# Kernel tuning notes

Measured on AMD Instinct MI355X. Metric: run time of the kernel, lower is better.

The kernel has to match this reference:

```python
import jax, jax.numpy as jnp
import numpy as np

K = 64          # tagset size (len(tag_to_ix))
START = 62      # start_tag_id
STOP = 63       # stop_tag_id
NEG = -10000.0


def setup_inputs() -> dict:
    key = jax.random.key(0)
    k1, k2, k3 = jax.random.split(key, 3)
    B, T = 1024, 512
    feats = jax.random.normal(k1, (B, T, K), dtype=jnp.float32)
    tags = jax.random.randint(k2, (B, T), 0, K, dtype=jnp.int32)
    # learned transition matrix; transitions[i, j] = score of moving from tag j to tag i
    transitions = jax.random.normal(k3, (K, K), dtype=jnp.float32)
    transitions = transitions.at[START, :].set(NEG).at[:, STOP].set(NEG)
    return {"feats": feats, "tags": tags, "transitions": transitions}


def reference(feats, tags, transitions):
    B, T, _ = feats.shape
    # log_alpha init: -10000 everywhere except start tag (matches torch code; feats[:,0] unused)
    alpha0 = jnp.full((B, K), NEG, dtype=feats.dtype).at[:, START].set(0.0)

    def step(alpha, feat_t):
        # alpha: [B, K]; new_alpha[b, i] = lse_j(transitions[i, j] + alpha[b, j]) + feat_t[b, i]
        new_alpha = jax.nn.logsumexp(transitions[None, :, :] + alpha[:, None, :], axis=-1) + feat_t
        return new_alpha, None

    feats_seq = jnp.transpose(feats[:, 1:, :], (1, 0, 2))  # [T-1, B, K]
    alpha, _ = jax.lax.scan(step, alpha0, feats_seq)
    forward_score = jax.nn.logsumexp(alpha, axis=-1)  # [B]

    # gold path score: sum_t transitions[tags[t], tags[t-1]] + feats[t, tags[t]], t = 1..T-1
    trans_score = transitions[tags[:, 1:], tags[:, :-1]].sum(axis=1)  # [B]
    emit_score = jnp.take_along_axis(feats[:, 1:, :], tags[:, 1:, None], axis=2)[..., 0].sum(axis=1)  # [B]
    gold_score = trans_score + emit_score

    return jnp.mean(forward_score - gold_score)
```

## Files before the change

kernel.cpp:

```cpp
#include <hip/hip_runtime.h>


#define BB 1024
#define TT 512
#define KK 64
#define START_TAG 62

#define RLF(v, l) __uint_as_float((unsigned)__builtin_amdgcn_readlane((int)__float_as_uint(v), (l)))

__global__ __launch_bounds__(128, 2) void crf_fwdbwd_kernel(
    const float* __restrict__ feats,
    const int*   __restrict__ tags,
    const float* __restrict__ trans,
    float*       __restrict__ diff)
{
  const int lane = threadIdx.x & 63;
  const int wv   = threadIdx.x >> 6;
  const int b    = blockIdx.x;

  __shared__ float ysh[KK];
  __shared__ float gs_sh;
  __shared__ int   esumB_sh;

  const float* fb = feats + (size_t)b * TT * KK + lane;

  float beta = 0.0f;
  int   esumA = 0;

  if (wv == 0) {
    float4 e4[16];
    {
      const float4* trow = (const float4*)(trans + lane * KK);
      #pragma unroll
      for (int jc = 0; jc < 16; ++jc) {
        float4 tv = trow[jc];
        e4[jc] = make_float4(__expf(tv.x), __expf(tv.y),
                             __expf(tv.z), __expf(tv.w));
      }
    }

    float upf[5];
    #pragma unroll
    for (int d = 0; d < 5; ++d) upf[d] = fb[(size_t)(1 + d) * KK];

    beta = (lane == START_TAG) ? 1.0f : 0.0f;
    float f_cur = __expf(upf[0]);

    for (int g = 0; g < 51; ++g) {
      #pragma unroll
      for (int d = 0; d < 5; ++d) {
        const int t = 1 + g * 5 + d;

        float4 a0 = {0.f, 0.f, 0.f, 0.f};
        float4 a1 = {0.f, 0.f, 0.f, 0.f};
        #pragma unroll
        for (int jc = 0; jc < 16; jc += 2) {
          a0.x = fmaf(e4[jc].x,     RLF(beta, 4*jc + 0), a0.x);
          a0.y = fmaf(e4[jc].y,     RLF(beta, 4*jc + 1), a0.y);
          a0.z = fmaf(e4[jc].z,     RLF(beta, 4*jc + 2), a0.z);
          a0.w = fmaf(e4[jc].w,     RLF(beta, 4*jc + 3), a0.w);
          a1.x = fmaf(e4[jc + 1].x, RLF(beta, 4*jc + 4), a1.x);
          a1.y = fmaf(e4[jc + 1].y, RLF(beta, 4*jc + 5), a1.y);
          a1.z = fmaf(e4[jc + 1].z, RLF(beta, 4*jc + 6), a1.z);
          a1.w = fmaf(e4[jc + 1].w, RLF(beta, 4*jc + 7), a1.w);
        }
        float z = ((a0.x + a1.x) + (a0.y + a1.y)) +
                  ((a0.z + a1.z) + (a0.w + a1.w));

        int tn = t + 5; if (tn > 255) tn = 255;
        upf[d] = fb[(size_t)tn * KK];

        unsigned zb = (unsigned)__builtin_amdgcn_readlane((int)__float_as_uint(z), 0);
        float s = __uint_as_float(0x7F000000u - (zb & 0x7F800000u));
        esumA += (int)((zb >> 23) & 0xFFu) - 127;
        beta = (z * f_cur) * s;

        f_cur = __expf(upf[(d + 1 < 5) ? d + 1 : 0]);
      }
    }
  } else {
    float4 et4[16];
    #pragma unroll
    for (int jc = 0; jc < 16; ++jc) {
      et4[jc].x = __expf(trans[(4*jc + 0) * KK + lane]);
      et4[jc].y = __expf(trans[(4*jc + 1) * KK + lane]);
      et4[jc].z = __expf(trans[(4*jc + 2) * KK + lane]);
      et4[jc].w = __expf(trans[(4*jc + 3) * KK + lane]);
    }

    float upf[4];
    #pragma unroll
    for (int d = 0; d < 4; ++d) upf[d] = fb[(size_t)(511 - d) * KK];

    float y = 1.0f;
    int esum = 0;
    float f_cur = __expf(upf[0]);

    for (int g = 0; g < 64; ++g) {
      #pragma unroll
      for (int d = 0; d < 4; ++d) {
        const int t = 511 - (g * 4 + d);

        float w = y * f_cur;
        float4 a0 = {0.f, 0.f, 0.f, 0.f};
        float4 a1 = {0.f, 0.f, 0.f, 0.f};
        #pragma unroll
        for (int jc = 0; jc < 16; jc += 2) {
          a0.x = fmaf(et4[jc].x,     RLF(w, 4*jc + 0), a0.x);
          a0.y = fmaf(et4[jc].y,     RLF(w, 4*jc + 1), a0.y);
          a0.z = fmaf(et4[jc].z,     RLF(w, 4*jc + 2), a0.z);
          a0.w = fmaf(et4[jc].w,     RLF(w, 4*jc + 3), a0.w);
          a1.x = fmaf(et4[jc + 1].x, RLF(w, 4*jc + 4), a1.x);
          a1.y = fmaf(et4[jc + 1].y, RLF(w, 4*jc + 5), a1.y);
          a1.z = fmaf(et4[jc + 1].z, RLF(w, 4*jc + 6), a1.z);
          a1.w = fmaf(et4[jc + 1].w, RLF(w, 4*jc + 7), a1.w);
        }
        float z = ((a0.x + a1.x) + (a0.y + a1.y)) +
                  ((a0.z + a1.z) + (a0.w + a1.w));

        int tn = t - 4; if (tn < 256) tn = 256;
        upf[d] = fb[(size_t)tn * KK];

        unsigned zb = (unsigned)__builtin_amdgcn_readlane((int)__float_as_uint(z), 0);
        float s = __uint_as_float(0x7F000000u - (zb & 0x7F800000u));
        esum += (int)((zb >> 23) & 0xFFu) - 127;
        y = z * s;

        f_cur = __expf(upf[(d + 1) & 3]);
      }
    }

    ysh[lane] = y;
    if (lane == 0) esumB_sh = esum;

    const int* tg = tags + b * TT;
    float gs = 0.0f;
    for (int tt = 1 + lane; tt < TT; tt += 64) {
      int tc = tg[tt];
      int tp = tg[tt - 1];
      gs += trans[tc * KK + tp]
          + feats[(size_t)b * TT * KK + (size_t)tt * KK + tc];
    }
    #pragma unroll
    for (int off = 32; off; off >>= 1) gs += __shfl_xor(gs, off);
    if (lane == 0) gs_sh = gs;
  }

  __syncthreads();

  if (wv == 0) {
    float p = beta * ysh[lane];
    #pragma unroll
    for (int off = 32; off; off >>= 1) p += __shfl_xor(p, off);
    float fwd = __logf(p) + (float)(esumA + esumB_sh) * 0.6931471805599453f;
    if (lane == 0) diff[b] = fwd - gs_sh;
  }
}

__global__ __launch_bounds__(1024) void reduce_mean_kernel(
    const float* __restrict__ diff, float* __restrict__ out)
{
  __shared__ float part[16];
  const int tid = threadIdx.x;
  float v = diff[tid];
  #pragma unroll
  for (int off = 32; off; off >>= 1) v += __shfl_xor(v, off);
  if ((tid & 63) == 0) part[tid >> 6] = v;
  __syncthreads();
  if (tid < 16) {
    float s = part[tid];
    #pragma unroll
    for (int off = 8; off; off >>= 1) s += __shfl_xor(s, off);
    if (tid == 0) out[0] = s * (1.0f / 1024.0f);
  }
}

extern "C" void kernel_launch(void* const* d_in, const int* in_sizes, int n_in,
                              void* d_out, int out_size, void* d_ws, size_t ws_size,
                              hipStream_t stream) {
  const float* feats = (const float*)d_in[0];
  const int*   tags  = (const int*)d_in[1];
  const float* trans = (const float*)d_in[2];
  float* out  = (float*)d_out;
  float* diff = (float*)d_ws;

  crf_fwdbwd_kernel<<<dim3(BB), dim3(128), 0, stream>>>(feats, tags, trans, diff);
  reduce_mean_kernel<<<dim3(1), dim3(1024), 0, stream>>>(diff, out);
}
```

Before: 260.0 us.

## Replace readlane broadcast matvec with DPP/shuffle XOR-permuted dot product

The 64x64 matrix-vector product in each recurrence step used to broadcast every element of the state vector with 64 scalar readlane operations. It now builds 16 lane-permuted copies using 3 cross-row shuffles and 12 DPP moves. The remaining permutations come from fused v_fmac_f32_dpp quad_perm instructions, with the transition matrix pre-permuted per lane by an XOR pattern to match. The aim is to remove the serialised readlane to SGPR to VALU dependency chain on the critical serial recurrence path, at the cost of inline asm with hazard nops and fragile permutation-index correctness.

```diff
diff --git a/kernel.cpp b/kernel.cpp
--- a/kernel.cpp
+++ b/kernel.cpp
@@ -6,9 +6,51 @@
 #define KK 64
 #define START_TAG 62
 
-#define RLF(v, l) __uint_as_float((unsigned)__builtin_amdgcn_readlane((int)__float_as_uint(v), (l)))
+#define RL0(v) ((unsigned)__builtin_amdgcn_readlane((int)__float_as_uint(v), 0))
 
-__global__ __launch_bounds__(128, 2) void crf_fwdbwd_kernel(
+#define DPPX(src, ctrl) __uint_as_float((unsigned)__builtin_amdgcn_update_dpp( \
+    0, (int)__float_as_uint(src), (ctrl), 0xF, 0xF, true))
+#define CTL_HM  0x141
+#define CTL_R8  0x128
+#define CTL_MIR 0x140
+
+#define FMQP1(acc, b, e) asm("v_fmac_f32_dpp %0, %1, %2 quad_perm:[1,0,3,2] row_mask:0xf bank_mask:0xf" : "+v"(acc) : "v"(b), "v"(e))
+#define FMQP2(acc, b, e) asm("v_fmac_f32_dpp %0, %1, %2 quad_perm:[2,3,0,1] row_mask:0xf bank_mask:0xf" : "+v"(acc) : "v"(b), "v"(e))
+#define FMQP3(acc, b, e) asm("v_fmac_f32_dpp %0, %1, %2 quad_perm:[3,2,1,0] row_mask:0xf bank_mask:0xf" : "+v"(acc) : "v"(b), "v"(e))
+
+__device__ __forceinline__ float xdot64(float bv, const float (&et)[64]) {
+  float cb00 = bv;
+  float cb10 = __shfl_xor(bv, 16);
+  float cb20 = __shfl_xor(bv, 32);
+  float cb30 = __shfl_xor(bv, 48);
+  float cb01 = DPPX(cb00, CTL_HM), cb02 = DPPX(cb00, CTL_R8), cb03 = DPPX(cb00, CTL_MIR);
+  float cb11 = DPPX(cb10, CTL_HM), cb12 = DPPX(cb10, CTL_R8), cb13 = DPPX(cb10, CTL_MIR);
+  float cb21 = DPPX(cb20, CTL_HM), cb22 = DPPX(cb20, CTL_R8), cb23 = DPPX(cb20, CTL_MIR);
+  float cb31 = DPPX(cb30, CTL_HM), cb32 = DPPX(cb30, CTL_R8), cb33 = DPPX(cb30, CTL_MIR);
+  float a0=0.f,a1=0.f,a2=0.f,a3=0.f,a4=0.f,a5=0.f,a6=0.f,a7=0.f;
+  __builtin_amdgcn_sched_barrier(0);
+  asm volatile("s_nop 1");
+  __builtin_amdgcn_sched_barrier(0);
+  a0 = fmaf(cb00, et[ 0], a0); FMQP1(a1, cb00, et[ 1]); FMQP2(a2, cb00, et[ 2]); FMQP3(a3, cb00, et[ 3]);
+  a4 = fmaf(cb01, et[ 4], a4); FMQP1(a5, cb01, et[ 5]); FMQP2(a6, cb01, et[ 6]); FMQP3(a7, cb01, et[ 7]);
+  a0 = fmaf(cb02, et[ 8], a0); FMQP1(a1, cb02, et[ 9]); FMQP2(a2, cb02, et[10]); FMQP3(a3, cb02, et[11]);
+  a4 = fmaf(cb03, et[12], a4); FMQP1(a5, cb03, et[13]); FMQP2(a6, cb03, et[14]); FMQP3(a7, cb03, et[15]);
+  a0 = fmaf(cb10, et[16], a0); FMQP1(a1, cb10, et[17]); FMQP2(a2, cb10, et[18]); FMQP3(a3, cb10, et[19]);
+  a4 = fmaf(cb11, et[20], a4); FMQP1(a5, cb11, et[21]); FMQP2(a6, cb11, et[22]); FMQP3(a7, cb11, et[23]);
+  a0 = fmaf(cb12, et[24], a0); FMQP1(a1, cb12, et[25]); FMQP2(a2, cb12, et[26]); FMQP3(a3, cb12, et[27]);
+  a4 = fmaf(cb13, et[28], a4); FMQP1(a5, cb13, et[29]); FMQP2(a6, cb13, et[30]); FMQP3(a7, cb13, et[31]);
+  a0 = fmaf(cb20, et[32], a0); FMQP1(a1, cb20, et[33]); FMQP2(a2, cb20, et[34]); FMQP3(a3, cb20, et[35]);
+  a4 = fmaf(cb21, et[36], a4); FMQP1(a5, cb21, et[37]); FMQP2(a6, cb21, et[38]); FMQP3(a7, cb21, et[39]);
+  a0 = fmaf(cb22, et[40], a0); FMQP1(a1, cb22, et[41]); FMQP2(a2, cb22, et[42]); FMQP3(a3, cb22, et[43]);
+  a4 = fmaf(cb23, et[44], a4); FMQP1(a5, cb23, et[45]); FMQP2(a6, cb23, et[46]); FMQP3(a7, cb23, et[47]);
+  a0 = fmaf(cb30, et[48], a0); FMQP1(a1, cb30, et[49]); FMQP2(a2, cb30, et[50]); FMQP3(a3, cb30, et[51]);
+  a4 = fmaf(cb31, et[52], a4); FMQP1(a5, cb31, et[53]); FMQP2(a6, cb31, et[54]); FMQP3(a7, cb31, et[55]);
+  a0 = fmaf(cb32, et[56], a0); FMQP1(a1, cb32, et[57]); FMQP2(a2, cb32, et[58]); FMQP3(a3, cb32, et[59]);
+  a4 = fmaf(cb33, et[60], a4); FMQP1(a5, cb33, et[61]); FMQP2(a6, cb33, et[62]); FMQP3(a7, cb33, et[63]);
+  return ((a0 + a4) + (a1 + a5)) + ((a2 + a6) + (a3 + a7));
+}
+
+__global__ __launch_bounds__(128, 2) void crf_dpp_kernel(
     const float* __restrict__ feats,
     const int*   __restrict__ tags,
     const float* __restrict__ trans,
@@ -23,20 +65,17 @@
   __shared__ int   esumB_sh;
 
   const float* fb = feats + (size_t)b * TT * KK + lane;
+  const int Bv[4] = {0, 7, 8, 15};
 
   float beta = 0.0f;
   int   esumA = 0;
 
   if (wv == 0) {
-    float4 e4[16];
-    {
-      const float4* trow = (const float4*)(trans + lane * KK);
-      #pragma unroll
-      for (int jc = 0; jc < 16; ++jc) {
-        float4 tv = trow[jc];
-        e4[jc] = make_float4(__expf(tv.x), __expf(tv.y),
-                             __expf(tv.z), __expf(tv.w));
-      }
+    float et[64];
+    #pragma unroll
+    for (int T = 0; T < 64; ++T) {
+      const int m = ((T >> 4) << 4) ^ Bv[(T >> 2) & 3] ^ (T & 3);
+      et[T] = __expf(trans[lane * KK + (lane ^ m)]);
     }
 
     float upf[5];
@@ -44,48 +83,32 @@
     for (int d = 0; d < 5; ++d) upf[d] = fb[(size_t)(1 + d) * KK];
 
     beta = (lane == START_TAG) ? 1.0f : 0.0f;
-    float f_cur = __expf(upf[0]);
+    float fA = __expf(upf[0]);
 
     for (int g = 0; g < 51; ++g) {
       #pragma unroll
       for (int d = 0; d < 5; ++d) {
         const int t = 1 + g * 5 + d;
 
-        float4 a0 = {0.f, 0.f, 0.f, 0.f};
-        float4 a1 = {0.f, 0.f, 0.f, 0.f};
-        #pragma unroll
-        for (int jc = 0; jc < 16; jc += 2) {
-          a0.x = fmaf(e4[jc].x,     RLF(beta, 4*jc + 0), a0.x);
-          a0.y = fmaf(e4[jc].y,     RLF(beta, 4*jc + 1), a0.y);
-          a0.z = fmaf(e4[jc].z,     RLF(beta, 4*jc + 2), a0.z);
-          a0.w = fmaf(e4[jc].w,     RLF(beta, 4*jc + 3), a0.w);
-          a1.x = fmaf(e4[jc + 1].x, RLF(beta, 4*jc + 4), a1.x);
-          a1.y = fmaf(e4[jc + 1].y, RLF(beta, 4*jc + 5), a1.y);
-          a1.z = fmaf(e4[jc + 1].z, RLF(beta, 4*jc + 6), a1.z);
-          a1.w = fmaf(e4[jc + 1].w, RLF(beta, 4*jc + 7), a1.w);
-        }
-        float z = ((a0.x + a1.x) + (a0.y + a1.y)) +
-                  ((a0.z + a1.z) + (a0.w + a1.w));
+        float zA = xdot64(beta, et);
 
         int tn = t + 5; if (tn > 255) tn = 255;
         upf[d] = fb[(size_t)tn * KK];
 
-        unsigned zb = (unsigned)__builtin_amdgcn_readlane((int)__float_as_uint(z), 0);
+        unsigned zb = RL0(zA);
         float s = __uint_as_float(0x7F000000u - (zb & 0x7F800000u));
         esumA += (int)((zb >> 23) & 0xFFu) - 127;
-        beta = (z * f_cur) * s;
+        beta = (zA * fA) * s;
 
-        f_cur = __expf(upf[(d + 1 < 5) ? d + 1 : 0]);
+        fA = __expf(upf[(d + 1 < 5) ? d + 1 : 0]);
       }
     }
   } else {
-    float4 et4[16];
+    float et[64];
     #pragma unroll
-    for (int jc = 0; jc < 16; ++jc) {
-      et4[jc].x = __expf(trans[(4*jc + 0) * KK + lane]);
-      et4[jc].y = __expf(trans[(4*jc + 1) * KK + lane]);
-      et4[jc].z = __expf(trans[(4*jc + 2) * KK + lane]);
-      et4[jc].w = __expf(trans[(4*jc + 3) * KK + lane]);
+    for (int T = 0; T < 64; ++T) {
+      const int m = ((T >> 4) << 4) ^ Bv[(T >> 2) & 3] ^ (T & 3);
+      et[T] = __expf(trans[(lane ^ m) * KK + lane]);
     }
 
     float upf[4];
@@ -94,39 +117,25 @@
 
     float y = 1.0f;
     int esum = 0;
-    float f_cur = __expf(upf[0]);
+    float fB = __expf(upf[0]);
 
     for (int g = 0; g < 64; ++g) {
       #pragma unroll
       for (int d = 0; d < 4; ++d) {
         const int t = 511 - (g * 4 + d);
 
-        float w = y * f_cur;
-        float4 a0 = {0.f, 0.f, 0.f, 0.f};
-        float4 a1 = {0.f, 0.f, 0.f, 0.f};
-        #pragma unroll
-        for (int jc = 0; jc < 16; jc += 2) {
-          a0.x = fmaf(et4[jc].x,     RLF(w, 4*jc + 0), a0.x);
-          a0.y = fmaf(et4[jc].y,     RLF(w, 4*jc + 1), a0.y);
-          a0.z = fmaf(et4[jc].z,     RLF(w, 4*jc + 2), a0.z);
-          a0.w = fmaf(et4[jc].w,     RLF(w, 4*jc + 3), a0.w);
-          a1.x = fmaf(et4[jc + 1].x, RLF(w, 4*jc + 4), a1.x);
-          a1.y = fmaf(et4[jc + 1].y, RLF(w, 4*jc + 5), a1.y);
-          a1.z = fmaf(et4[jc + 1].z, RLF(w, 4*jc + 6), a1.z);
-          a1.w = fmaf(et4[jc + 1].w, RLF(w, 4*jc + 7), a1.w);
-        }
-        float z = ((a0.x + a1.x) + (a0.y + a1.y)) +
-                  ((a0.z + a1.z) + (a0.w + a1.w));
+        float w = y * fB;
+        float zB = xdot64(w, et);
 
         int tn = t - 4; if (tn < 256) tn = 256;
         upf[d] = fb[(size_t)tn * KK];
 
-        unsigned zb = (unsigned)__builtin_amdgcn_readlane((int)__float_as_uint(z), 0);
+        unsigned zb = RL0(zB);
         float s = __uint_as_float(0x7F000000u - (zb & 0x7F800000u));
         esum += (int)((zb >> 23) & 0xFFu) - 127;
-        y = z * s;
+        y = zB * s;
 
-        f_cur = __expf(upf[(d + 1) & 3]);
+        fB = __expf(upf[(d + 1) & 3]);
       }
     }
 
@@ -184,6 +193,6 @@
   float* out  = (float*)d_out;
   float* diff = (float*)d_ws;
 
-  crf_fwdbwd_kernel<<<dim3(BB), dim3(128), 0, stream>>>(feats, tags, trans, diff);
+  crf_dpp_kernel<<<dim3(BB), dim3(128), 0, stream>>>(feats, tags, trans, diff);
   reduce_mean_kernel<<<dim3(1), dim3(1024), 0, stream>>>(diff, out);
 }
```

Measured after the change: 253.7 us. 1.02x faster.
